# Performance work log

Hardware: AMD Instinct MI355X
Metric: run time of the kernel (lower is better)

Reference implementation:

```python
import jax, jax.numpy as jnp
import numpy as np
from jax.scipy.special import erf

N = 128          # n_points
STEPS = 64       # number of velocity steps
MAX_TIME = 100.0
E = 4096         # number of events
P = 4000         # number of unique node pairs
DELTA = MAX_TIME / (STEPS - 1)  # time_delta_size
EPS = 1e-9


def setup_inputs() -> dict:
    key = jax.random.key(0)
    k1, k2, k3 = jax.random.split(key, 3)
    beta = jnp.ones((1, 1), jnp.float32)
    z0 = jax.random.uniform(k1, (N, 2), jnp.float32) * 0.5
    v0 = jax.random.uniform(k2, (N, 2, STEPS), jnp.float32) * 0.5
    # event times strictly inside [0, max_time) so floor(t/DELTA) < STEPS
    event_times = jax.random.uniform(k3, (E,), jnp.float32, 0.0, MAX_TIME * 0.999)
    # unique upper-triangular node pairs (torch.unique on data[:,0:2] hoisted to setup)
    rng = np.random.default_rng(0)
    iu, ju = np.triu_indices(N, k=1)
    sel = rng.choice(iu.shape[0], size=P, replace=False)
    pairs_i = jnp.asarray(iu[sel], jnp.int32)
    pairs_j = jnp.asarray(ju[sel], jnp.int32)
    t0 = jnp.zeros((1,), jnp.float32)
    tn = jnp.full((1,), MAX_TIME, jnp.float32)
    return {"beta": beta, "z0": z0, "v0": v0, "event_times": event_times,
            "t0": t0, "tn": tn, "pairs_i": pairs_i, "pairs_j": pairs_j}


def reference(beta, z0, v0, event_times, t0, tn, pairs_i, pairs_j):
    dtype = z0.dtype
    # time_deltas = cat([0], diff(linspace(0, max_time, steps)))  -> (STEPS,)
    time_deltas = jnp.concatenate(
        [jnp.zeros((1,), dtype), jnp.full((STEPS - 1,), DELTA, dtype)])
    b = beta[0, 0]

    # steps(): per-step starting positions  Z_steps[n, c, s] = z0 + v0 * dt_s
    Z_steps = z0[:, :, None] + v0 * time_deltas              # (N, 2, STEPS)

    # gather time-step latents for each event time
    tv = event_times / DELTA                                 # (E,)
    tf = jnp.floor(tv)
    frac = tv - tf                                           # fractional step offset
    idx = jnp.clip(tf.astype(jnp.int32), 0, STEPS - 1)       # (E,)
    Zt = Z_steps[:, :, idx] + v0[:, :, idx] * frac           # (N, 2, E)

    # event term: sum over unique pairs of (beta - ||z_i(t) - z_j(t)||^2)
    Zi = Zt[pairs_i]                                         # (P, 2, E)
    Zj = Zt[pairs_j]
    d_pairs = jnp.sum((Zi - Zj) ** 2, axis=1)                # (P, E)
    event_intensity = jnp.sum(b - d_pairs)

    # non-event term: analytical integral of exp(beta - ||dz + dv*u||^2)
    # over each step duration, summed over steps, upper triangle only
    dz = Z_steps[:, None] - Z_steps[None, :]                 # (N, N, 2, STEPS)
    dv = v0[:, None] - v0[None, :]                           # (N, N, 2, STEPS)
    r2 = jnp.sum(dv * dv, axis=2) + EPS                      # (N, N, STEPS)
    r = jnp.sqrt(r2)
    zdv = jnp.sum(dz * dv, axis=2)
    bshift = zdv / r2
    c = jnp.sum(dz * dz, axis=2) - zdv * zdv / r2
    integ = (jnp.exp(b - c) * (jnp.sqrt(jnp.pi) / (2.0 * r))
             * (erf(r * (time_deltas + bshift)) - erf(r * bshift)))  # (N,N,STEPS)
    mat = jnp.sum(integ, axis=2)                             # (N, N)
    mask = jnp.triu(jnp.ones((N, N), bool), k=1)
    non_event_intensity = jnp.sum(jnp.where(mask, mat, jnp.zeros((), dtype)))

    return event_intensity - non_event_intensity
```

## Files before the change

### kernel.cpp

```cpp
#include <hip/hip_runtime.h>

#define NPTS   128
#define NSTEPS 64
#define NEV    4096
#define NPAIR  4000
#define DELTA_F (100.0f / 63.0f)
#define EPSF    1e-9f
#define SQRTPI_OVER2 0.88622692545275801365f

#define WS_ACCUM_OFF 0
#define WS_S1_OFF    16
#define WS_S2_OFF    (16 + 64 * 4)
#define WS_TOTAL_BYTES (16 + 64 * 4 * 2)

__device__ __forceinline__ void block_reduce_atomic(float v, double* target) {
    #pragma unroll
    for (int off = 32; off > 0; off >>= 1) v += __shfl_down(v, off, 64);
    __shared__ float ws[4];
    int lane = threadIdx.x & 63;
    int wid  = threadIdx.x >> 6;
    if (lane == 0) ws[wid] = v;
    __syncthreads();
    if (threadIdx.x == 0) {
        float tot = ws[0] + ws[1] + ws[2] + ws[3];
        atomicAdd(target, (double)tot);
    }
}

__global__ void stats_kernel(const float* __restrict__ event_times,
                             float* __restrict__ S1, float* __restrict__ S2) {
    __shared__ float s1[NSTEPS], s2[NSTEPS];
    int t = threadIdx.x;
    if (t < NSTEPS) { s1[t] = 0.f; s2[t] = 0.f; }
    __syncthreads();
    for (int e = t; e < NEV; e += blockDim.x) {
        float tv = event_times[e] / DELTA_F;
        float tf = floorf(tv);
        float f  = tv - tf;
        int s = (int)tf;
        s = s < 0 ? 0 : (s > NSTEPS - 1 ? NSTEPS - 1 : s);
        float a = (s == 0 ? 0.f : DELTA_F) + f;
        atomicAdd(&s1[s], a);
        atomicAdd(&s2[s], a * a);
    }
    __syncthreads();
    if (t < NSTEPS) { S1[t] = s1[t]; S2[t] = s2[t]; }
}

__global__ void event_kernel(const float* __restrict__ z0,
                             const float* __restrict__ v0,
                             const int*   __restrict__ pi,
                             const int*   __restrict__ pj,
                             const float* __restrict__ S1,
                             const float* __restrict__ S2,
                             double* __restrict__ accum) {
    const int total = NPAIR * NSTEPS;
    float local = 0.f;
    for (int idx = blockIdx.x * blockDim.x + threadIdx.x; idx < total;
         idx += gridDim.x * blockDim.x) {
        int s = idx & (NSTEPS - 1);
        int p = idx >> 6;
        int i = pi[p], j = pj[p];
        float dz0x = z0[i * 2 + 0] - z0[j * 2 + 0];
        float dz0y = z0[i * 2 + 1] - z0[j * 2 + 1];
        float dvx = v0[(i * 2 + 0) * NSTEPS + s] - v0[(j * 2 + 0) * NSTEPS + s];
        float dvy = v0[(i * 2 + 1) * NSTEPS + s] - v0[(j * 2 + 1) * NSTEPS + s];
        float Q1 = dz0x * dvx + dz0y * dvy;
        float Q2 = dvx * dvx + dvy * dvy;
        float term = 2.f * S1[s] * Q1 + S2[s] * Q2;
        if (s == 0) {
            term += (float)NEV * (dz0x * dz0x + dz0y * dz0y);
        }
        local += term;
    }
    block_reduce_atomic(local, accum + 0);
}

__global__ void nonevent_kernel(const float* __restrict__ beta,
                                const float* __restrict__ z0,
                                const float* __restrict__ v0,
                                double* __restrict__ accum) {
    const float b = beta[0];
    const int total = NPTS * NPTS * NSTEPS;
    float local = 0.f;
    for (int idx = blockIdx.x * blockDim.x + threadIdx.x; idx < total;
         idx += gridDim.x * blockDim.x) {
        int s  = idx & (NSTEPS - 1);
        int ij = idx >> 6;
        int i  = ij >> 7;
        int j  = ij & (NPTS - 1);
        if (j > i) {
            float td = (s == 0) ? 0.f : DELTA_F;
            float vix = v0[(i * 2 + 0) * NSTEPS + s];
            float viy = v0[(i * 2 + 1) * NSTEPS + s];
            float vjx = v0[(j * 2 + 0) * NSTEPS + s];
            float vjy = v0[(j * 2 + 1) * NSTEPS + s];
            float dvx = vix - vjx;
            float dvy = viy - vjy;
            float dzx = (z0[i * 2 + 0] - z0[j * 2 + 0]) + dvx * td;
            float dzy = (z0[i * 2 + 1] - z0[j * 2 + 1]) + dvy * td;
            float r2  = dvx * dvx + dvy * dvy + EPSF;
            float r   = sqrtf(r2);
            float zdv = dzx * dvx + dzy * dvy;
            float bsh = zdv / r2;
            float cc  = dzx * dzx + dzy * dzy - zdv * zdv / r2;
            float integ = expf(b - cc) * (SQRTPI_OVER2 / r) *
                          (erff(r * (td + bsh)) - erff(r * bsh));
            local += integ;
        }
    }
    block_reduce_atomic(local, accum + 1);
}

__global__ void finalize_kernel(const float* __restrict__ beta,
                                const double* __restrict__ accum,
                                float* __restrict__ out) {
    double ev = (double)beta[0] * (double)NPAIR * (double)NEV - accum[0];
    out[0] = (float)(ev - accum[1]);
}

extern "C" void kernel_launch(void* const* d_in, const int* in_sizes, int n_in,
                              void* d_out, int out_size, void* d_ws, size_t ws_size,
                              hipStream_t stream) {
    const float* beta        = (const float*)d_in[0];
    const float* z0          = (const float*)d_in[1];
    const float* v0          = (const float*)d_in[2];
    const float* event_times = (const float*)d_in[3];
    const int* pairs_i = (const int*)d_in[6];
    const int* pairs_j = (const int*)d_in[7];
    float* out = (float*)d_out;

    char* ws = (char*)d_ws;
    double* accum = (double*)(ws + WS_ACCUM_OFF);
    float*  S1    = (float*)(ws + WS_S1_OFF);
    float*  S2    = (float*)(ws + WS_S2_OFF);

    hipMemsetAsync(d_ws, 0, WS_TOTAL_BYTES, stream);

    stats_kernel<<<1, 256, 0, stream>>>(event_times, S1, S2);
    event_kernel<<<512, 256, 0, stream>>>(z0, v0, pairs_i, pairs_j, S1, S2, accum);
    nonevent_kernel<<<1024, 256, 0, stream>>>(beta, z0, v0, accum);
    finalize_kernel<<<1, 1, 0, stream>>>(beta, accum, out);
}
```

Before: 102.6 us.

## Fuse stats, event and non-event kernels into one launch with per-block partials

Merges the event-time histogram, event term and non-event term into a single kernel. Each block redundantly recomputes the per-step S1/S2 sums in shared memory and caches z0 in shared memory. The memset and double atomics are replaced by per-block partial sums that a 64-thread finalize kernel reduces. This cuts launch count and serialization. In exchange every block re-reads all 4096 event times, and the grid shrinks to 256 blocks, so each thread handles more of the non-event work.

Result: faster. 88.54 us (-13.7%).

```diff
diff --git a/kernel.cpp b/kernel.cpp
--- a/kernel.cpp
+++ b/kernel.cpp
@@ -8,32 +8,26 @@
 #define EPSF    1e-9f
 #define SQRTPI_OVER2 0.88622692545275801365f
 
-#define WS_ACCUM_OFF 0
-#define WS_S1_OFF    16
-#define WS_S2_OFF    (16 + 64 * 4)
-#define WS_TOTAL_BYTES (16 + 64 * 4 * 2)
+#define GRID 256
+#define BLK  256
 
-__device__ __forceinline__ void block_reduce_atomic(float v, double* target) {
-    #pragma unroll
-    for (int off = 32; off > 0; off >>= 1) v += __shfl_down(v, off, 64);
-    __shared__ float ws[4];
-    int lane = threadIdx.x & 63;
-    int wid  = threadIdx.x >> 6;
-    if (lane == 0) ws[wid] = v;
+
+__global__ __launch_bounds__(BLK) void fused_kernel(
+    const float* __restrict__ beta,
+    const float* __restrict__ z0,
+    const float* __restrict__ v0,
+    const float* __restrict__ event_times,
+    const int*   __restrict__ pi,
+    const int*   __restrict__ pj,
+    float* __restrict__ partials) {
+    __shared__ float s1[NSTEPS], s2[NSTEPS];
+    __shared__ float zsh[NPTS * 2];
+    const int t = threadIdx.x;
+
+    if (t < NSTEPS) { s1[t] = 0.f; s2[t] = 0.f; }
+    zsh[t] = z0[t];
     __syncthreads();
-    if (threadIdx.x == 0) {
-        float tot = ws[0] + ws[1] + ws[2] + ws[3];
-        atomicAdd(target, (double)tot);
-    }
-}
-
-__global__ void stats_kernel(const float* __restrict__ event_times,
-                             float* __restrict__ S1, float* __restrict__ S2) {
-    __shared__ float s1[NSTEPS], s2[NSTEPS];
-    int t = threadIdx.x;
-    if (t < NSTEPS) { s1[t] = 0.f; s2[t] = 0.f; }
-    __syncthreads();
-    for (int e = t; e < NEV; e += blockDim.x) {
+    for (int e = t; e < NEV; e += BLK) {
         float tv = event_times[e] / DELTA_F;
         float tf = floorf(tv);
         float f  = tv - tf;
@@ -44,79 +38,80 @@
         atomicAdd(&s2[s], a * a);
     }
     __syncthreads();
-    if (t < NSTEPS) { S1[t] = s1[t]; S2[t] = s2[t]; }
-}
 
-__global__ void event_kernel(const float* __restrict__ z0,
-                             const float* __restrict__ v0,
-                             const int*   __restrict__ pi,
-                             const int*   __restrict__ pj,
-                             const float* __restrict__ S1,
-                             const float* __restrict__ S2,
-                             double* __restrict__ accum) {
-    const int total = NPAIR * NSTEPS;
-    float local = 0.f;
-    for (int idx = blockIdx.x * blockDim.x + threadIdx.x; idx < total;
-         idx += gridDim.x * blockDim.x) {
+    const float b = beta[0];
+
+    float lev = 0.f;
+    for (int idx = blockIdx.x * BLK + t; idx < NPAIR * NSTEPS; idx += GRID * BLK) {
         int s = idx & (NSTEPS - 1);
         int p = idx >> 6;
         int i = pi[p], j = pj[p];
-        float dz0x = z0[i * 2 + 0] - z0[j * 2 + 0];
-        float dz0y = z0[i * 2 + 1] - z0[j * 2 + 1];
+        float dz0x = zsh[i * 2 + 0] - zsh[j * 2 + 0];
+        float dz0y = zsh[i * 2 + 1] - zsh[j * 2 + 1];
         float dvx = v0[(i * 2 + 0) * NSTEPS + s] - v0[(j * 2 + 0) * NSTEPS + s];
         float dvy = v0[(i * 2 + 1) * NSTEPS + s] - v0[(j * 2 + 1) * NSTEPS + s];
         float Q1 = dz0x * dvx + dz0y * dvy;
         float Q2 = dvx * dvx + dvy * dvy;
-        float term = 2.f * S1[s] * Q1 + S2[s] * Q2;
-        if (s == 0) {
-            term += (float)NEV * (dz0x * dz0x + dz0y * dz0y);
-        }
-        local += term;
+        float term = 2.f * s1[s] * Q1 + s2[s] * Q2;
+        if (s == 0) term += (float)NEV * (dz0x * dz0x + dz0y * dz0y);
+        lev += term;
     }
-    block_reduce_atomic(local, accum + 0);
-}
 
-__global__ void nonevent_kernel(const float* __restrict__ beta,
-                                const float* __restrict__ z0,
-                                const float* __restrict__ v0,
-                                double* __restrict__ accum) {
-    const float b = beta[0];
-    const int total = NPTS * NPTS * NSTEPS;
-    float local = 0.f;
-    for (int idx = blockIdx.x * blockDim.x + threadIdx.x; idx < total;
-         idx += gridDim.x * blockDim.x) {
+    float lne = 0.f;
+    for (int idx = blockIdx.x * BLK + t; idx < NPTS * NPTS * NSTEPS; idx += GRID * BLK) {
         int s  = idx & (NSTEPS - 1);
         int ij = idx >> 6;
         int i  = ij >> 7;
         int j  = ij & (NPTS - 1);
         if (j > i) {
             float td = (s == 0) ? 0.f : DELTA_F;
-            float vix = v0[(i * 2 + 0) * NSTEPS + s];
-            float viy = v0[(i * 2 + 1) * NSTEPS + s];
-            float vjx = v0[(j * 2 + 0) * NSTEPS + s];
-            float vjy = v0[(j * 2 + 1) * NSTEPS + s];
-            float dvx = vix - vjx;
-            float dvy = viy - vjy;
-            float dzx = (z0[i * 2 + 0] - z0[j * 2 + 0]) + dvx * td;
-            float dzy = (z0[i * 2 + 1] - z0[j * 2 + 1]) + dvy * td;
+            float dvx = v0[(i * 2 + 0) * NSTEPS + s] - v0[(j * 2 + 0) * NSTEPS + s];
+            float dvy = v0[(i * 2 + 1) * NSTEPS + s] - v0[(j * 2 + 1) * NSTEPS + s];
+            float dzx = (zsh[i * 2 + 0] - zsh[j * 2 + 0]) + dvx * td;
+            float dzy = (zsh[i * 2 + 1] - zsh[j * 2 + 1]) + dvy * td;
             float r2  = dvx * dvx + dvy * dvy + EPSF;
             float r   = sqrtf(r2);
             float zdv = dzx * dvx + dzy * dvy;
             float bsh = zdv / r2;
             float cc  = dzx * dzx + dzy * dzy - zdv * zdv / r2;
-            float integ = expf(b - cc) * (SQRTPI_OVER2 / r) *
-                          (erff(r * (td + bsh)) - erff(r * bsh));
-            local += integ;
+            lne += expf(b - cc) * (SQRTPI_OVER2 / r) *
+                   (erff(r * (td + bsh)) - erff(r * bsh));
         }
     }
-    block_reduce_atomic(local, accum + 1);
+
+    #pragma unroll
+    for (int off = 32; off > 0; off >>= 1) {
+        lev += __shfl_down(lev, off, 64);
+        lne += __shfl_down(lne, off, 64);
+    }
+    __shared__ float wsv[4], wsn[4];
+    int lane = t & 63, wid = t >> 6;
+    if (lane == 0) { wsv[wid] = lev; wsn[wid] = lne; }
+    __syncthreads();
+    if (t == 0) {
+        partials[blockIdx.x]        = wsv[0] + wsv[1] + wsv[2] + wsv[3];
+        partials[GRID + blockIdx.x] = wsn[0] + wsn[1] + wsn[2] + wsn[3];
+    }
 }
 
 __global__ void finalize_kernel(const float* __restrict__ beta,
-                                const double* __restrict__ accum,
+                                const float* __restrict__ partials,
                                 float* __restrict__ out) {
-    double ev = (double)beta[0] * (double)NPAIR * (double)NEV - accum[0];
-    out[0] = (float)(ev - accum[1]);
+    int lane = threadIdx.x;
+    double ev = 0.0, ne = 0.0;
+    for (int k = lane; k < GRID; k += 64) {
+        ev += (double)partials[k];
+        ne += (double)partials[GRID + k];
+    }
+    #pragma unroll
+    for (int off = 32; off > 0; off >>= 1) {
+        ev += __shfl_down(ev, off, 64);
+        ne += __shfl_down(ne, off, 64);
+    }
+    if (lane == 0) {
+        double evt = (double)beta[0] * (double)NPAIR * (double)NEV - ev;
+        out[0] = (float)(evt - ne);
+    }
 }
 
 extern "C" void kernel_launch(void* const* d_in, const int* in_sizes, int n_in,
@@ -129,16 +124,9 @@
     const int* pairs_i = (const int*)d_in[6];
     const int* pairs_j = (const int*)d_in[7];
     float* out = (float*)d_out;
+    float* partials = (float*)d_ws;
 
-    char* ws = (char*)d_ws;
-    double* accum = (double*)(ws + WS_ACCUM_OFF);
-    float*  S1    = (float*)(ws + WS_S1_OFF);
-    float*  S2    = (float*)(ws + WS_S2_OFF);
-
-    hipMemsetAsync(d_ws, 0, WS_TOTAL_BYTES, stream);
-
-    stats_kernel<<<1, 256, 0, stream>>>(event_times, S1, S2);
-    event_kernel<<<512, 256, 0, stream>>>(z0, v0, pairs_i, pairs_j, S1, S2, accum);
-    nonevent_kernel<<<1024, 256, 0, stream>>>(beta, z0, v0, accum);
-    finalize_kernel<<<1, 1, 0, stream>>>(beta, accum, out);
+    fused_kernel<<<GRID, BLK, 0, stream>>>(beta, z0, v0, event_times,
+                                           pairs_i, pairs_j, partials);
+    finalize_kernel<<<1, 64, 0, stream>>>(beta, partials, out);
 }
```
